# Kernel optimization log

Measured on AMD Instinct MI355X. Metric: run time of the kernel, lower is better.

## Reference

```python
import jax, jax.numpy as jnp
import numpy as np

THETA = 10000.0
EPS = 1e-6

def _rope_tables(n, d):
    # 2D image RoPE: square grid side x side, half of head-dim rotates with
    # row position, half with column position. rotate-half pairing (i, i+d/2).
    side = int(np.sqrt(n))
    dq = d // 4  # angle count per spatial axis
    inv_freq = 1.0 / (THETA ** (np.arange(dq, dtype=np.float32) / dq))
    ang = np.arange(side, dtype=np.float32)[:, None] * inv_freq[None, :]  # [side, dq]
    row = np.broadcast_to(ang[:, None, :], (side, side, dq)).reshape(n, dq)
    col = np.broadcast_to(ang[None, :, :], (side, side, dq)).reshape(n, dq)
    angles = np.concatenate([row, col], axis=-1)  # [n, d//2]
    return jnp.asarray(np.cos(angles)), jnp.asarray(np.sin(angles))

def _apply_rope(t, cos, sin):
    # t: [b, h, n, d]; cos/sin: [n, d//2]
    d2 = t.shape[-1] // 2
    t1, t2 = t[..., :d2], t[..., d2:]
    return jnp.concatenate([t1 * cos - t2 * sin, t1 * sin + t2 * cos], axis=-1)

def _rmsnorm(t, scale):
    var = jnp.mean(t * t, axis=-1, keepdims=True)
    return t * jax.lax.rsqrt(var + EPS) * scale

def setup_inputs() -> dict:
    key = jax.random.key(0)
    ks = jax.random.split(key, 3)
    B, N, D = 8, 1024, 1024
    x = jax.random.normal(ks[0], (B, N, D), dtype=jnp.float32)
    Wqkv = jax.random.normal(ks[1], (D, 3 * D), dtype=jnp.float32) * (D ** -0.5)
    bqkv = jnp.zeros((3 * D,), dtype=jnp.float32)
    Wout = jax.random.normal(ks[2], (D, D), dtype=jnp.float32) * (D ** -0.5)
    bout = jnp.zeros((D,), dtype=jnp.float32)
    hd = D // 16
    return {"x": x, "Wqkv": Wqkv, "bqkv": bqkv, "Wout": Wout, "bout": bout,
            "q_scale": jnp.ones((hd,), jnp.float32), "k_scale": jnp.ones((hd,), jnp.float32)}

def reference(x, Wqkv, bqkv, Wout, bout, q_scale, k_scale):
    B, N, D = x.shape
    H = 16
    hd = D // H
    qkv = x @ Wqkv + bqkv  # [B, N, 3D]
    qkv = qkv.reshape(B, N, 3, H, hd).transpose(2, 0, 3, 1, 4)  # [3, B, H, N, hd]
    q, k, v = qkv[0], qkv[1], qkv[2]
    q = _rmsnorm(q, q_scale)
    k = _rmsnorm(k, k_scale)
    cos, sin = _rope_tables(N, hd)
    q = _apply_rope(q, cos, sin)
    k = _apply_rope(k, cos, sin)
    scale = hd ** -0.5
    scores = jnp.einsum('bhqd,bhkd->bhqk', q, k) * scale
    attn = jax.nn.softmax(scores, axis=-1)
    o = jnp.einsum('bhqk,bhkd->bhqd', attn, v)  # [B, H, N, hd]
    o = o.transpose(0, 2, 1, 3).reshape(B, N, D)
    return o @ Wout + bout
```

## Files before the change

kernel.cpp:

```cpp
#include <hip/hip_runtime.h>
#include <hip/hip_bf16.h>
#include <hip/hip_fp16.h>
#include <math.h>

#define QSZ 8388608

typedef short bf16x8 __attribute__((ext_vector_type(8)));
typedef _Float16 f16x8 __attribute__((ext_vector_type(8)));
typedef float f32x4 __attribute__((ext_vector_type(4)));

__device__ __forceinline__ unsigned short f2bf(float f) {
  __hip_bfloat16 h = __float2bfloat16(f);
  return *reinterpret_cast<unsigned short*>(&h);
}

__device__ __forceinline__ void gload16(const void* g, void* l) {
  __builtin_amdgcn_global_load_lds(
      (const __attribute__((address_space(1))) void*)g,
      (__attribute__((address_space(3))) void*)l, 16, 0, 0);
}

__global__ __launch_bounds__(256)
void cvt_bf16(const float* __restrict__ src, unsigned short* __restrict__ dst) {
  const int i = (blockIdx.x * 256 + threadIdx.x) * 8;
  const float4 a = *(const float4*)&src[i];
  const float4 b = *(const float4*)&src[i + 4];
  ushort4 lo, hi;
  lo.x = f2bf(a.x); lo.y = f2bf(a.y); lo.z = f2bf(a.z); lo.w = f2bf(a.w);
  hi.x = f2bf(b.x); hi.y = f2bf(b.y); hi.z = f2bf(b.z); hi.w = f2bf(b.w);
  *(ushort4*)&dst[i] = lo;
  *(ushort4*)&dst[i + 4] = hi;
}

__global__ __launch_bounds__(256)
void cvt_t(const float* __restrict__ src, unsigned short* __restrict__ dst,
           const int N) {
  __shared__ unsigned short tile[32][33];
  const int k0 = blockIdx.y * 32, n0 = blockIdx.x * 32;
  const int t = threadIdx.x;
  const int r = t >> 3, c4 = (t & 7) * 4;
  const float4 v = *(const float4*)&src[(k0 + r) * N + n0 + c4];
  tile[r][c4 + 0] = f2bf(v.x);
  tile[r][c4 + 1] = f2bf(v.y);
  tile[r][c4 + 2] = f2bf(v.z);
  tile[r][c4 + 3] = f2bf(v.w);
  __syncthreads();
  ushort4 o;
  o.x = tile[c4 + 0][r];
  o.y = tile[c4 + 1][r];
  o.z = tile[c4 + 2][r];
  o.w = tile[c4 + 3][r];
  *(ushort4*)&dst[(long)(n0 + r) * 1024 + k0 + c4] = o;
}

__global__ __launch_bounds__(512, 2)
void gemm_qkv(const unsigned short* __restrict__ A,
              const unsigned short* __restrict__ Bt,
              const float* __restrict__ bias,
              __half* __restrict__ Ch,
              const float* __restrict__ qsc,
              const float* __restrict__ ksc) {
  __shared__ __align__(16) unsigned short As[2][16384];
  __shared__ __align__(16) unsigned short Bs[2][16384];
  __shared__ float2 Tab[512];

  const int t = threadIdx.x;
  const int swz = (blockIdx.x & 7) * 48 + (blockIdx.x >> 3);
  const int bm = swz / 12, bn = swz % 12;
  const int w = t >> 6, lane = t & 63;
  const int M0 = (w >> 2) * 128, N0 = (w & 3) * 64;
  const int lm = lane & 15, q4 = lane >> 4;

  {
    const int pos = t >> 4, idx = t & 15;
    const float invf = expf(-(float)idx * 0.57564627324851149f);
    const float ang = (float)pos * invf;
    Tab[t] = make_float2(cosf(ang), sinf(ang));
  }

  const int c8 = ((t & 7) ^ ((t >> 3) & 7)) << 3;
  const unsigned short* aSrc = A + (long)(bm * 256 + (t >> 3)) * 1024 + c8;
  const unsigned short* bSrc = Bt + (long)(bn * 256 + (t >> 3)) * 1024 + c8;
  unsigned short* lA[2] = {&As[0][t * 8], &As[1][t * 8]};
  unsigned short* lB[2] = {&Bs[0][t * 8], &Bs[1][t * 8]};

  f32x4 acc[8][4] = {};

  auto stage = [&](int buf, int kt) {
    const unsigned short* a = aSrc + kt * 64;
    const unsigned short* b = bSrc + kt * 64;
    unsigned short* la = lA[buf];
    unsigned short* lb = lB[buf];
#pragma unroll
    for (int j = 0; j < 4; ++j) {
      gload16(a + j * 65536, la + j * 4096);
      gload16(b + j * 65536, lb + j * 4096);
    }
  };

  auto compute = [&](const unsigned short* Ac, const unsigned short* Bc) {
#pragma unroll
    for (int kk = 0; kk < 2; ++kk) {
      bf16x8 af[8], bg[4];
#pragma unroll
      for (int mi = 0; mi < 8; ++mi) {
        const int row = M0 + mi * 16 + lm;
        af[mi] = *(const bf16x8*)
            &Ac[row * 64 + ((((kk << 2) + q4) ^ (row & 7)) << 3)];
      }
#pragma unroll
      for (int ni = 0; ni < 4; ++ni) {
        const int row = N0 + ni * 16 + lm;
        bg[ni] = *(const bf16x8*)
            &Bc[row * 64 + ((((kk << 2) + q4) ^ (row & 7)) << 3)];
      }
#pragma unroll
      for (int mi = 0; mi < 8; ++mi)
#pragma unroll
        for (int ni = 0; ni < 4; ++ni)
          acc[mi][ni] = __builtin_amdgcn_mfma_f32_16x16x32_bf16(
              af[mi], bg[ni], acc[mi][ni], 0, 0, 0);
    }
  };

  stage(0, 0);
  stage(1, 1);
  asm volatile("s_waitcnt vmcnt(8)" ::: "memory");
  __builtin_amdgcn_s_barrier();

  for (int kt = 0; kt < 14; ++kt) {
    const int s = kt & 1;
    compute(s ? &As[1][0] : &As[0][0], s ? &Bs[1][0] : &Bs[0][0]);
    asm volatile("s_waitcnt lgkmcnt(0)" ::: "memory");
    __builtin_amdgcn_s_barrier();
    stage(s, kt + 2);
    asm volatile("s_waitcnt vmcnt(8)" ::: "memory");
    __builtin_amdgcn_s_barrier();
  }
  compute(&As[0][0], &Bs[0][0]);
  asm volatile("s_waitcnt lgkmcnt(0)" ::: "memory");
  __builtin_amdgcn_s_barrier();
  asm volatile("s_waitcnt vmcnt(0)" ::: "memory");
  __builtin_amdgcn_s_barrier();
  compute(&As[1][0], &Bs[1][0]);

  const int r0 = q4 << 2;
  const int nb = bn * 256 + N0;
  const int tq = nb >> 10, h = (nb >> 6) & 15;

  if (tq == 2) {
#pragma unroll
    for (int mi = 0; mi < 8; ++mi)
#pragma unroll
      for (int ni = 0; ni < 4; ++ni) {
        const int col = nb + ni * 16 + lm;
        const int dd = col & 63;
        const float bv = bias[col];
#pragma unroll
        for (int r = 0; r < 4; ++r) {
          const int m = bm * 256 + M0 + mi * 16 + r0 + r;
          const int b = m >> 10, nn = m & 1023;
          Ch[2L * QSZ + ((long)((b * 16 + h) * 64 + dd)) * 1024 + nn] =
              __float2half(acc[mi][ni][r] + bv);
        }
      }
    return;
  }

  const float* scp = (tq == 0) ? qsc : ksc;
  const float qmul = (tq == 0) ? 0.18033688011112042f : 1.0f;
  float scv[4], bv[4];
#pragma unroll
  for (int ni = 0; ni < 4; ++ni) {
    scv[ni] = scp[ni * 16 + lm];
    bv[ni] = bias[nb + ni * 16 + lm];
  }
  __half* base = Ch + (long)tq * QSZ;
#pragma unroll
  for (int mi = 0; mi < 8; ++mi) {
#pragma unroll
    for (int r = 0; r < 4; ++r) {
      const float v0 = acc[mi][0][r] + bv[0];
      const float v1 = acc[mi][1][r] + bv[1];
      const float v2 = acc[mi][2][r] + bv[2];
      const float v3 = acc[mi][3][r] + bv[3];
      float ss = v0 * v0 + v1 * v1 + v2 * v2 + v3 * v3;
      ss += __shfl_xor(ss, 1, 64);
      ss += __shfl_xor(ss, 2, 64);
      ss += __shfl_xor(ss, 4, 64);
      ss += __shfl_xor(ss, 8, 64);
      const float inv = rsqrtf(ss * (1.0f / 64.0f) + 1e-6f) * qmul;
      const float a0 = v0 * inv * scv[0];
      const float a1 = v1 * inv * scv[1];
      const float a2 = v2 * inv * scv[2];
      const float a3 = v3 * inv * scv[3];
      const int m = bm * 256 + M0 + mi * 16 + r0 + r;
      const int b = m >> 10, nn = m & 1023;
      const float2 tr = Tab[(nn >> 5) * 16 + lm];
      const float2 tc = Tab[(nn & 31) * 16 + lm];
      __half* row = base + ((long)((b * 16 + h) * 1024 + nn)) * 64 + lm;
      row[0]  = __float2half(a0 * tr.x - a2 * tr.y);
      row[16] = __float2half(a1 * tc.x - a3 * tc.y);
      row[32] = __float2half(a0 * tr.y + a2 * tr.x);
      row[48] = __float2half(a1 * tc.y + a3 * tc.x);
    }
  }
}

template<int MODE, int GX>
__global__ __launch_bounds__(256)
void gemm_bf16(const unsigned short* __restrict__ A,
               const unsigned short* __restrict__ Bt,
               const float* __restrict__ bias, float* __restrict__ Cf,
               __half* __restrict__ Ch, const float* __restrict__ qsc,
               const float* __restrict__ ksc) {
  __shared__ __align__(16) unsigned short As[2][4096];
  __shared__ __align__(16) unsigned short Bs[2][4096];
  const int t = threadIdx.x;
  const int flat = blockIdx.x + blockIdx.y * GX;
  const int xcd = flat & 7, j = flat >> 3;
  const int bm = xcd * 8 + (j & 7), bn = j >> 3;
  const int w = t >> 6, lane = t & 63;
  const int wm = (w & 1) << 6, wn = (w >> 1) << 6;
  const int lm = lane & 15, lk = (lane >> 4) << 3;

  const unsigned short* aptr =
      A + (long)(bm * 128 + (t >> 2)) * 1024 + ((t & 3) << 3);
  const unsigned short* bptr =
      Bt + (long)(bn * 128 + (t >> 2)) * 1024 + ((t & 3) << 3);

  f32x4 acc[4][4] = {};

  gload16(aptr, &As[0][t * 8]);
  gload16(aptr + 64 * 1024, &As[0][2048 + t * 8]);
  gload16(bptr, &Bs[0][t * 8]);
  gload16(bptr + 64 * 1024, &Bs[0][2048 + t * 8]);

  for (int it = 0; it < 32; ++it) {
    const int cur = it & 1;
    __syncthreads();
    if (it < 31) {
      const int nx = cur ^ 1;
      const int kk = (it + 1) * 32;
      gload16(aptr + kk, &As[nx][t * 8]);
      gload16(aptr + 64 * 1024 + kk, &As[nx][2048 + t * 8]);
      gload16(bptr + kk, &Bs[nx][t * 8]);
      gload16(bptr + 64 * 1024 + kk, &Bs[nx][2048 + t * 8]);
    }
    bf16x8 af[4], bfr[4];
#pragma unroll
    for (int mi = 0; mi < 4; ++mi)
      af[mi] = *(const bf16x8*)&As[cur][(wm + mi * 16 + lm) * 32 + lk];
#pragma unroll
    for (int ni = 0; ni < 4; ++ni)
      bfr[ni] = *(const bf16x8*)&Bs[cur][(wn + ni * 16 + lm) * 32 + lk];
#pragma unroll
    for (int mi = 0; mi < 4; ++mi)
#pragma unroll
      for (int ni = 0; ni < 4; ++ni)
        acc[mi][ni] = __builtin_amdgcn_mfma_f32_16x16x32_bf16(
            af[mi], bfr[ni], acc[mi][ni], 0, 0, 0);
  }

  const int r0 = (lane >> 4) << 2;
  const int nb = bn * 128 + wn;

#pragma unroll
  for (int mi = 0; mi < 4; ++mi)
#pragma unroll
    for (int ni = 0; ni < 4; ++ni) {
      const int n = nb + ni * 16 + lm;
      const float bvv = bias[n];
#pragma unroll
      for (int r = 0; r < 4; ++r)
        Cf[(long)(bm * 128 + wm + mi * 16 + r0 + r) * 1024 + n] =
            acc[mi][ni][r] + bvv;
    }
}

__global__ __launch_bounds__(256, 3)
void attn_mfma(const __half* __restrict__ qh, const __half* __restrict__ kh,
               const __half* __restrict__ vh, unsigned short* __restrict__ ob) {
  __shared__ __align__(16) __half Ks[2][4096];
  __shared__ __align__(16) __half Vs[2][4096];
  __shared__ __align__(16) __half Pl[8][1152];
  const int t = threadIdx.x;
  const int w = t >> 6, lane = t & 63;
  const int flat = blockIdx.x + blockIdx.y * 8;
  const int xcd = flat & 7, j = flat >> 3;
  const int bh = xcd * 16 + (j >> 3);
  const int qt = j & 7;
  const int lm = lane & 15, q4 = lane >> 4;

  f16x8 qf[2][2];
#pragma unroll
  for (int g = 0; g < 2; ++g) {
    const __half* qrow =
        qh + ((long)(bh * 1024 + qt * 128 + g * 64 + w * 16 + lm)) * 64 +
        q4 * 8;
    qf[g][0] = *(const f16x8*)qrow;
    qf[g][1] = *(const f16x8*)(qrow + 32);
  }

  f32x4 o[2][4] = {};
  float l_r[2][4] = {};

  const int prow = t >> 3, pc = t & 7;
  const int scz = pc ^ (prow & 7);
  const __half* ksrc0 = kh + (long)(bh * 1024 + prow) * 64 + scz * 8;
  const __half* vsrc0 = vh + (long)(bh * 64 + prow) * 1024 + scz * 8;

  gload16(ksrc0, &Ks[0][t * 8]);
  gload16(ksrc0 + 32 * 64, &Ks[0][2048 + t * 8]);
  gload16(vsrc0, &Vs[0][t * 8]);
  gload16(vsrc0 + 32 * 1024, &Vs[0][2048 + t * 8]);

  for (int kc = 0; kc < 16; ++kc) {
    const int cur = kc & 1;
    __syncthreads();

    if (kc < 15) {
      const int nx = cur ^ 1;
      const __half* ksrc = ksrc0 + (kc + 1) * 4096;
      const __half* vsrc = vsrc0 + (kc + 1) * 64;
      gload16(ksrc, &Ks[nx][t * 8]);
      gload16(ksrc + 32 * 64, &Ks[nx][2048 + t * 8]);
      gload16(vsrc, &Vs[nx][t * 8]);
      gload16(vsrc + 32 * 1024, &Vs[nx][2048 + t * 8]);
    }

    f16x8 kf[4][2];
#pragma unroll
    for (int nt = 0; nt < 4; ++nt) {
      const int kr = nt * 16 + lm;
#pragma unroll
      for (int ks = 0; ks < 2; ++ks)
        kf[nt][ks] = *(const f16x8*)&Ks[cur][kr * 64 +
                                      (((ks << 2) + q4) ^ (kr & 7)) * 8];
    }

#pragma unroll
    for (int g = 0; g < 2; ++g) {
      f32x4 s[4];
      __builtin_amdgcn_s_setprio(1);
#pragma unroll
      for (int nt = 0; nt < 4; ++nt) {
        s[nt] = (f32x4){0.f, 0.f, 0.f, 0.f};
#pragma unroll
        for (int ks = 0; ks < 2; ++ks)
          s[nt] = __builtin_amdgcn_mfma_f32_16x16x32_f16(qf[g][ks], kf[nt][ks],
                                                         s[nt], 0, 0, 0);
      }
      __builtin_amdgcn_s_setprio(0);
      __half* Pw = &Pl[w * 2 + g][0];
#pragma unroll
      for (int nt = 0; nt < 4; ++nt) {
#pragma unroll
        for (int r = 0; r < 4; ++r) {
          const float p = exp2f(s[nt][r] - 12.98425536800067f);
          l_r[g][r] += p;
          Pw[(q4 * 4 + r) * 72 + nt * 16 + lm] = (__half)p;
        }
      }
    }

    __builtin_amdgcn_s_setprio(1);
#pragma unroll
    for (int ks2 = 0; ks2 < 2; ++ks2) {
      const f16x8 pf0 = *(const f16x8*)&Pl[w * 2 + 0][lm * 72 + ks2 * 32 +
                                                      q4 * 8];
      const f16x8 pf1 = *(const f16x8*)&Pl[w * 2 + 1][lm * 72 + ks2 * 32 +
                                                      q4 * 8];
#pragma unroll
      for (int nt = 0; nt < 4; ++nt) {
        const int dr = nt * 16 + lm;
        const f16x8 vf = *(const f16x8*)&Vs[cur][dr * 64 +
                                          (((ks2 << 2) + q4) ^ (dr & 7)) * 8];
        o[0][nt] = __builtin_amdgcn_mfma_f32_16x16x32_f16(pf0, vf, o[0][nt],
                                                          0, 0, 0);
        o[1][nt] = __builtin_amdgcn_mfma_f32_16x16x32_f16(pf1, vf, o[1][nt],
                                                          0, 0, 0);
      }
    }
    __builtin_amdgcn_s_setprio(0);
  }

  const int b = bh >> 4, h = bh & 15;
#pragma unroll
  for (int g = 0; g < 2; ++g) {
#pragma unroll
    for (int r = 0; r < 4; ++r) {
      float l = l_r[g][r];
      l += __shfl_xor(l, 1, 64);
      l += __shfl_xor(l, 2, 64);
      l += __shfl_xor(l, 4, 64);
      l += __shfl_xor(l, 8, 64);
      const float linv = 1.0f / l;
      const long rowg =
          (long)(b * 1024 + qt * 128 + g * 64 + w * 16 + q4 * 4 + r) * 1024 +
          h * 64;
#pragma unroll
      for (int nt = 0; nt < 4; ++nt)
        ob[rowg + nt * 16 + lm] = f2bf(o[g][nt][r] * linv);
    }
  }
}

extern "C" void kernel_launch(void* const* d_in, const int* in_sizes, int n_in,
                              void* d_out, int out_size, void* d_ws,
                              size_t ws_size, hipStream_t stream) {
  const float* x    = (const float*)d_in[0];
  const float* Wqkv = (const float*)d_in[1];
  const float* bqkv = (const float*)d_in[2];
  const float* Wout = (const float*)d_in[3];
  const float* bout = (const float*)d_in[4];
  const float* qs   = (const float*)d_in[5];
  const float* ks   = (const float*)d_in[6];
  float* out = (float*)d_out;
  float* W = (float*)d_ws;

  __half* qkvh = (__half*)W;
  __half* qpre = qkvh;
  __half* kpre = qkvh + QSZ;
  __half* vT   = qkvh + 2 * QSZ;
  unsigned short* xb  = (unsigned short*)(W + 12582912);
  unsigned short* ob  = xb;
  unsigned short* wqT = (unsigned short*)(W + 16777216);
  unsigned short* woT = wqT + 3 * 1024 * 1024;

  cvt_bf16<<<4096, 256, 0, stream>>>(x, xb);
  cvt_t<<<dim3(96, 32), 256, 0, stream>>>(Wqkv, wqT, 3072);
  cvt_t<<<dim3(32, 32), 256, 0, stream>>>(Wout, woT, 1024);
  gemm_qkv<<<384, 512, 0, stream>>>(xb, wqT, bqkv, qkvh, qs, ks);
  attn_mfma<<<dim3(8, 128), 256, 0, stream>>>(qpre, kpre, vT, ob);
  gemm_bf16<1, 8><<<dim3(8, 64), 256, 0, stream>>>(ob, woT, bout, out, nullptr,
                                                   nullptr, nullptr);
}
```

Before: 269.0 us.

## Restructure QKV GEMM main loop into four-slot half-K pipeline with interleaved loads

The QKV projection GEMM's K loop now runs over 32-wide half tiles held in a four-slot LDS ring instead of a double buffer of 64-wide tiles. Each quarter of work issues part of the next global-to-LDS copy between fragment reads and MFMA bursts, and MFMA sections run at raised wave priority. The aim is to hide global load latency and LDS reads behind matrix math, in the style of ping-pong schedules. The cost is many more barriers per iteration, and the manual vmcnt accounting has to stay correct for the deeper prefetch.

```diff
diff --git a/kernel.cpp b/kernel.cpp
--- a/kernel.cpp
+++ b/kernel.cpp
@@ -60,8 +60,8 @@
               __half* __restrict__ Ch,
               const float* __restrict__ qsc,
               const float* __restrict__ ksc) {
-  __shared__ __align__(16) unsigned short As[2][16384];
-  __shared__ __align__(16) unsigned short Bs[2][16384];
+  __shared__ __align__(16) unsigned short HA[4][8192];
+  __shared__ __align__(16) unsigned short HB[4][8192];
   __shared__ float2 Tab[512];
 
   const int t = threadIdx.x;
@@ -78,71 +78,109 @@
     Tab[t] = make_float2(cosf(ang), sinf(ang));
   }
 
-  const int c8 = ((t & 7) ^ ((t >> 3) & 7)) << 3;
-  const unsigned short* aSrc = A + (long)(bm * 256 + (t >> 3)) * 1024 + c8;
-  const unsigned short* bSrc = Bt + (long)(bn * 256 + (t >> 3)) * 1024 + c8;
-  unsigned short* lA[2] = {&As[0][t * 8], &As[1][t * 8]};
-  unsigned short* lB[2] = {&Bs[0][t * 8], &Bs[1][t * 8]};
+  const int c8 = (((t & 3) ^ ((t >> 2) & 3)) << 3);
+  const unsigned short* aSrc = A + (long)(bm * 256 + (t >> 2)) * 1024 + c8;
+  const unsigned short* bSrc = Bt + (long)(bn * 256 + (t >> 2)) * 1024 + c8;
 
   f32x4 acc[8][4] = {};
 
-  auto stage = [&](int buf, int kt) {
-    const unsigned short* a = aSrc + kt * 64;
-    const unsigned short* b = bSrc + kt * 64;
-    unsigned short* la = lA[buf];
-    unsigned short* lb = lB[buf];
-#pragma unroll
-    for (int j = 0; j < 4; ++j) {
-      gload16(a + j * 65536, la + j * 4096);
-      gload16(b + j * 65536, lb + j * 4096);
-    }
-  };
-
-  auto compute = [&](const unsigned short* Ac, const unsigned short* Bc) {
-#pragma unroll
-    for (int kk = 0; kk < 2; ++kk) {
-      bf16x8 af[8], bg[4];
-#pragma unroll
-      for (int mi = 0; mi < 8; ++mi) {
-        const int row = M0 + mi * 16 + lm;
-        af[mi] = *(const bf16x8*)
-            &Ac[row * 64 + ((((kk << 2) + q4) ^ (row & 7)) << 3)];
-      }
-#pragma unroll
-      for (int ni = 0; ni < 4; ++ni) {
-        const int row = N0 + ni * 16 + lm;
-        bg[ni] = *(const bf16x8*)
-            &Bc[row * 64 + ((((kk << 2) + q4) ^ (row & 7)) << 3)];
-      }
-#pragma unroll
-      for (int mi = 0; mi < 8; ++mi)
-#pragma unroll
-        for (int ni = 0; ni < 4; ++ni)
-          acc[mi][ni] = __builtin_amdgcn_mfma_f32_16x16x32_bf16(
-              af[mi], bg[ni], acc[mi][ni], 0, 0, 0);
-    }
-  };
-
-  stage(0, 0);
-  stage(1, 1);
+  auto stageA = [&](int G) {
+    const unsigned short* a = aSrc + ((G >> 1) << 6) + ((G & 1) << 5);
+    unsigned short* la = &HA[G & 3][t * 8];
+    gload16(a, la);
+    gload16(a + 128 * 1024, la + 4096);
+  };
+  auto stageB = [&](int G) {
+    const unsigned short* b = bSrc + ((G >> 1) << 6) + ((G & 1) << 5);
+    unsigned short* lb = &HB[G & 3][t * 8];
+    gload16(b, lb);
+    gload16(b + 128 * 1024, lb + 4096);
+  };
+
+  auto rdA4 = [&](bf16x8* dst, int slot, int mi0) {
+#pragma unroll
+    for (int i = 0; i < 4; ++i) {
+      const int r = M0 + (mi0 + i) * 16 + lm;
+      dst[i] = *(const bf16x8*)&HA[slot][r * 32 + ((q4 ^ (lm & 3)) << 3)];
+    }
+  };
+  auto rdB4 = [&](bf16x8* dst, int slot) {
+#pragma unroll
+    for (int i = 0; i < 4; ++i) {
+      const int r = N0 + i * 16 + lm;
+      dst[i] = *(const bf16x8*)&HB[slot][r * 32 + ((q4 ^ (lm & 3)) << 3)];
+    }
+  };
+  auto mfmaQ = [&](const bf16x8* fa, const bf16x8* fb, int mb) {
+    __builtin_amdgcn_s_setprio(1);
+#pragma unroll
+    for (int mi = 0; mi < 4; ++mi)
+#pragma unroll
+      for (int ni = 0; ni < 4; ++ni)
+        acc[mb + mi][ni] = __builtin_amdgcn_mfma_f32_16x16x32_bf16(
+            fa[mi], fb[ni], acc[mb + mi][ni], 0, 0, 0);
+    __builtin_amdgcn_s_setprio(0);
+  };
+  auto bar = [] { __builtin_amdgcn_s_barrier(); };
+  auto lgkm0 = [] {
+    asm volatile("s_waitcnt lgkmcnt(0)" ::: "memory");
+    __builtin_amdgcn_sched_barrier(0);
+  };
+
+  stageA(0); stageB(0);
+  stageA(1); stageB(1);
+  stageA(2); stageB(2);
   asm volatile("s_waitcnt vmcnt(8)" ::: "memory");
-  __builtin_amdgcn_s_barrier();
-
+  bar();
+
+  bf16x8 fa[4], fb[4], fa2[4];
   for (int kt = 0; kt < 14; ++kt) {
-    const int s = kt & 1;
-    compute(s ? &As[1][0] : &As[0][0], s ? &Bs[1][0] : &Bs[0][0]);
-    asm volatile("s_waitcnt lgkmcnt(0)" ::: "memory");
-    __builtin_amdgcn_s_barrier();
-    stage(s, kt + 2);
+    const int h0 = (2 * kt) & 3, h1 = (2 * kt + 1) & 3;
+    rdA4(fa, h0, 0); rdB4(fb, h0);
+    stageA(2 * kt + 3);
+    bar(); lgkm0(); mfmaQ(fa, fb, 0); bar();
+    rdA4(fa2, h0, 4);
+    stageB(2 * kt + 3);
+    bar(); lgkm0(); mfmaQ(fa2, fb, 4);
     asm volatile("s_waitcnt vmcnt(8)" ::: "memory");
-    __builtin_amdgcn_s_barrier();
-  }
-  compute(&As[0][0], &Bs[0][0]);
-  asm volatile("s_waitcnt lgkmcnt(0)" ::: "memory");
-  __builtin_amdgcn_s_barrier();
-  asm volatile("s_waitcnt vmcnt(0)" ::: "memory");
-  __builtin_amdgcn_s_barrier();
-  compute(&As[1][0], &Bs[1][0]);
+    bar();
+    rdA4(fa, h1, 0); rdB4(fb, h1);
+    stageA(2 * kt + 4);
+    bar(); lgkm0(); mfmaQ(fa, fb, 0); bar();
+    rdA4(fa2, h1, 4);
+    stageB(2 * kt + 4);
+    bar(); lgkm0(); mfmaQ(fa2, fb, 4);
+    asm volatile("s_waitcnt vmcnt(8)" ::: "memory");
+    bar();
+  }
+  {
+    rdA4(fa, 0, 0); rdB4(fb, 0);
+    stageA(31);
+    bar(); lgkm0(); mfmaQ(fa, fb, 0); bar();
+    rdA4(fa2, 0, 4);
+    stageB(31);
+    bar(); lgkm0(); mfmaQ(fa2, fb, 4);
+    asm volatile("s_waitcnt vmcnt(8)" ::: "memory");
+    bar();
+    rdA4(fa, 1, 0); rdB4(fb, 1);
+    bar(); lgkm0(); mfmaQ(fa, fb, 0); bar();
+    rdA4(fa2, 1, 4);
+    bar(); lgkm0(); mfmaQ(fa2, fb, 4);
+    asm volatile("s_waitcnt vmcnt(4)" ::: "memory");
+    bar();
+  }
+  {
+    rdA4(fa, 2, 0); rdB4(fb, 2);
+    bar(); lgkm0(); mfmaQ(fa, fb, 0); bar();
+    rdA4(fa2, 2, 4);
+    bar(); lgkm0(); mfmaQ(fa2, fb, 4);
+    asm volatile("s_waitcnt vmcnt(0)" ::: "memory");
+    bar();
+    rdA4(fa, 3, 0); rdB4(fb, 3);
+    bar(); lgkm0(); mfmaQ(fa, fb, 0); bar();
+    rdA4(fa2, 3, 4);
+    bar(); lgkm0(); mfmaQ(fa2, fb, 4);
+  }
 
   const int r0 = q4 << 2;
   const int nb = bn * 256 + N0;
```

New measurement: 275.9 us. +2.6%, slower.
